# Optimization experiments

Measured on AMD Instinct MI355X. Metric: run time of the kernel, lower is better.

## Reference

```python
import jax, jax.numpy as jnp
import numpy as np

H = 64  # hidden_dim

def _rnn_layer(x, Wih, Whh, bih, bhh):
    # x: [B, T, D_in] -> hidden states [B, T, H]; PyTorch RNN tanh cell:
    # h_t = tanh(W_ih x_t + b_ih + W_hh h_{t-1} + b_hh)
    B = x.shape[0]
    xp = jnp.einsum('btd,hd->bth', x, Wih) + bih  # precompute input projection
    h0 = jnp.zeros((B, H), dtype=x.dtype)
    def step(h, xt):
        h = jnp.tanh(xt + h @ Whh.T + bhh)
        return h, h
    _, hs = jax.lax.scan(step, h0, jnp.swapaxes(xp, 0, 1))  # scan over T
    return jnp.swapaxes(hs, 0, 1)  # [B, T, H]

def setup_inputs() -> dict:
    key = jax.random.key(0)
    ks = jax.random.split(key, 14)
    B, T, D = 4096, 512, 1
    s = 0.1  # small init scale to keep tanh unsaturated
    inp = {
        'x': jax.random.normal(ks[0], (B, T, D), dtype=jnp.float32),
        'W_ih0': jax.random.normal(ks[1], (H, D), dtype=jnp.float32) * s,
        'W_hh0': jax.random.normal(ks[2], (H, H), dtype=jnp.float32) * s,
        'b_ih0': jax.random.normal(ks[3], (H,), dtype=jnp.float32) * s,
        'b_hh0': jax.random.normal(ks[4], (H,), dtype=jnp.float32) * s,
        'W_ih1': jax.random.normal(ks[5], (H, H), dtype=jnp.float32) * s,
        'W_hh1': jax.random.normal(ks[6], (H, H), dtype=jnp.float32) * s,
        'b_ih1': jax.random.normal(ks[7], (H,), dtype=jnp.float32) * s,
        'b_hh1': jax.random.normal(ks[8], (H,), dtype=jnp.float32) * s,
        'fc1_W': jax.random.normal(ks[9], (64, H), dtype=jnp.float32) * s,
        'fc1_b': jax.random.normal(ks[10], (64,), dtype=jnp.float32) * s,
        'fc2_W': jax.random.normal(ks[11], (1, 64), dtype=jnp.float32) * s,
        'fc2_b': jax.random.normal(ks[12], (1,), dtype=jnp.float32) * s,
    }
    return inp

def reference(x, W_ih0, W_hh0, b_ih0, b_hh0, W_ih1, W_hh1, b_ih1, b_hh1,
              fc1_W, fc1_b, fc2_W, fc2_b):
    h1 = _rnn_layer(x, W_ih0, W_hh0, b_ih0, b_hh0)   # layer 0
    h2 = _rnn_layer(h1, W_ih1, W_hh1, b_ih1, b_hh1)  # layer 1
    last = h2[:, -1, :]                               # [B, H]
    z = jax.nn.relu(last @ fc1_W.T + fc1_b)
    return z @ fc2_W.T + fc2_b                        # [B, 1]
```

## Files before the change

### kernel.cpp

```cpp
#include <hip/hip_runtime.h>

namespace {

constexpr int T_LEN = 512;
constexpr int XS    = 516;

typedef _Float16 half8  __attribute__((ext_vector_type(8)));
typedef float    f32x4v __attribute__((ext_vector_type(4)));
typedef unsigned uint2v __attribute__((ext_vector_type(2)));
typedef unsigned uint4v __attribute__((ext_vector_type(4)));

#define MFMA32(a, b, c) __builtin_amdgcn_mfma_f32_16x16x32_f16((a), (b), (c), 0, 0, 0)

constexpr float SCL = 2.8853900817779268f;

__device__ __forceinline__ float exp2_fast(float x) {
#if __has_builtin(__builtin_amdgcn_exp2f)
    return __builtin_amdgcn_exp2f(x);
#else
    return exp2f(x);
#endif
}

__device__ __forceinline__ half8 load_frag(const float* __restrict__ W,
                                           int row, int k0, float s) {
    const float* p = W + row * 64 + k0;
    f32x4v lo = *reinterpret_cast<const f32x4v*>(p);
    f32x4v hi = *reinterpret_cast<const f32x4v*>(p + 4);
    uint4v u;
    u.x = __builtin_bit_cast(unsigned, __builtin_amdgcn_cvt_pkrtz(lo.x * s, lo.y * s));
    u.y = __builtin_bit_cast(unsigned, __builtin_amdgcn_cvt_pkrtz(lo.z * s, lo.w * s));
    u.z = __builtin_bit_cast(unsigned, __builtin_amdgcn_cvt_pkrtz(hi.x * s, hi.y * s));
    u.w = __builtin_bit_cast(unsigned, __builtin_amdgcn_cvt_pkrtz(hi.z * s, hi.w * s));
    return __builtin_bit_cast(half8, u);
}

__device__ __forceinline__ void tanh4(f32x4v &a) {
#pragma unroll
    for (int q = 0; q < 4; ++q) {
        float e = exp2_fast(a[q]);
        a[q] = 1.0f - 2.0f * __builtin_amdgcn_rcpf(e + 1.0f);
    }
}

__device__ __forceinline__ int swz_off(int b, int ro) {
    const int chunk = ro >> 3;
    const int within = ro & 7;
    return (b << 6) + (((chunk ^ (b & 7))) << 3) + within;
}

__global__ __launch_bounds__(256, 2)
void rnn_swz_kernel(const float* __restrict__ x,
                    const float* __restrict__ Wih0,
                    const float* __restrict__ Whh0,
                    const float* __restrict__ bih0,
                    const float* __restrict__ bhh0,
                    const float* __restrict__ Wih1,
                    const float* __restrict__ Whh1,
                    const float* __restrict__ bih1,
                    const float* __restrict__ bhh1,
                    const float* __restrict__ fc1W,
                    const float* __restrict__ fc1b,
                    const float* __restrict__ fc2W,
                    const float* __restrict__ fc2b,
                    float* __restrict__ out)
{
    const int tid    = threadIdx.x;
    const int wv     = tid >> 6;
    const int lane   = tid & 63;
    const int g      = lane >> 4;
    const int b16    = lane & 15;
    const int batch0 = blockIdx.x * 16;

    __shared__ float    sx[16 * XS];
    __shared__ _Float16 sh1[2][16 * 64];
    __shared__ _Float16 sh2[2][16 * 64];
    __shared__ float    pf[4][16];

    {
        const float* gx = x + (size_t)batch0 * T_LEN;
#pragma unroll
        for (int c = 0; c < 8; ++c) {
            int idx = tid + c * 256;
            int r = idx >> 7, c4 = idx & 127;
            f32x4v v = *reinterpret_cast<const f32x4v*>(gx + r * T_LEN + c4 * 4);
            *reinterpret_cast<f32x4v*>(&sx[r * XS + c4 * 4]) = v;
        }
    }

    const int row = 16 * wv + b16;
    const int ro  = 16 * wv + 4 * g;

    const half8 WA0_0 = load_frag(Whh0, row,      8 * g, SCL);
    const half8 WA0_1 = load_frag(Whh0, row, 32 + 8 * g, SCL);
    const half8 WI1_0 = load_frag(Wih1, row,      8 * g, SCL);
    const half8 WI1_1 = load_frag(Wih1, row, 32 + 8 * g, SCL);
    const half8 WH1_0 = load_frag(Whh1, row,      8 * g, SCL);
    const half8 WH1_1 = load_frag(Whh1, row, 32 + 8 * g, SCL);

    f32x4v bb0, bb1, wx2;
#pragma unroll
    for (int q = 0; q < 4; ++q) {
        const int o = 16 * wv + 4 * g + q;
        bb0[q] = SCL * (bih0[o] + bhh0[o]);
        bb1[q] = SCL * (bih1[o] + bhh1[o]);
        wx2[q] = SCL * Wih0[o];
    }

    const int wr_off = swz_off(b16, ro);
    const int rd_b0  = swz_off(b16, 8 * g);
    const int rd_b1  = swz_off(b16, 32 + 8 * g);

    auto publish = [&](_Float16* base, const f32x4v& a) {
        uint2v p;
        p.x = __builtin_bit_cast(unsigned, __builtin_amdgcn_cvt_pkrtz(a[0], a[1]));
        p.y = __builtin_bit_cast(unsigned, __builtin_amdgcn_cvt_pkrtz(a[2], a[3]));
        *reinterpret_cast<uint2v*>(base + wr_off) = p;
    };

    half8 Bh1_0, Bh1_1, Bh2_0, Bh2_1;

    __syncthreads();

    float xt = sx[b16 * XS + 0];
    float xn = sx[b16 * XS + 1];

    {
        f32x4v a0 = wx2 * xt + bb0;
        tanh4(a0);
        publish(sh1[0], a0);
        *reinterpret_cast<uint2v*>(&sh2[0][0] + wr_off) = uint2v{0, 0};
        __syncthreads();
        Bh1_0 = *reinterpret_cast<const half8*>(&sh1[0][0] + rd_b0);
        Bh1_1 = *reinterpret_cast<const half8*>(&sh1[0][0] + rd_b1);
        Bh2_0 = *reinterpret_cast<const half8*>(&sh2[0][0] + rd_b0);
        Bh2_1 = *reinterpret_cast<const half8*>(&sh2[0][0] + rd_b1);
        xt = xn; xn = sx[b16 * XS + 2];
    }

#pragma unroll 2
    for (int k = 1; k < T_LEN; ++k) {
        const int s = k & 1;
        const float xf = sx[b16 * XS + k + 2];

        f32x4v zz = {};
        f32x4v u0 = MFMA32(WA0_0, Bh1_0, wx2 * xt + bb0);
        f32x4v v0 = MFMA32(WA0_1, Bh1_1, zz);
        f32x4v u1 = MFMA32(WI1_0, Bh1_0, bb1);
        f32x4v v1 = MFMA32(WH1_0, Bh2_0, zz);
        u1 = MFMA32(WI1_1, Bh1_1, u1);
        v1 = MFMA32(WH1_1, Bh2_1, v1);

        f32x4v a0 = u0 + v0;
        tanh4(a0);
        publish(sh1[s], a0);

        f32x4v a1 = u1 + v1;
        tanh4(a1);
        publish(sh2[s], a1);

        __syncthreads();
        Bh1_0 = *reinterpret_cast<const half8*>(&sh1[s][0] + rd_b0);
        Bh1_1 = *reinterpret_cast<const half8*>(&sh1[s][0] + rd_b1);
        Bh2_0 = *reinterpret_cast<const half8*>(&sh2[s][0] + rd_b0);
        Bh2_1 = *reinterpret_cast<const half8*>(&sh2[s][0] + rd_b1);
        xt = xn; xn = xf;
    }

    {
        f32x4v zz = {};
        f32x4v u1 = MFMA32(WI1_0, Bh1_0, bb1);
        f32x4v v1 = MFMA32(WH1_0, Bh2_0, zz);
        u1 = MFMA32(WI1_1, Bh1_1, u1);
        v1 = MFMA32(WH1_1, Bh2_1, v1);
        f32x4v a1 = u1 + v1;
        tanh4(a1);
        publish(sh2[0], a1);
        __syncthreads();
        Bh2_0 = *reinterpret_cast<const half8*>(&sh2[0][0] + rd_b0);
        Bh2_1 = *reinterpret_cast<const half8*>(&sh2[0][0] + rd_b1);
    }

    {
        const half8 F0 = load_frag(fc1W, row,      8 * g, 1.0f);
        const half8 F1 = load_frag(fc1W, row, 32 + 8 * g, 1.0f);
        f32x4v zf;
#pragma unroll
        for (int q = 0; q < 4; ++q) zf[q] = fc1b[16 * wv + 4 * g + q];
        zf = MFMA32(F0, Bh2_0, zf);
        zf = MFMA32(F1, Bh2_1, zf);

        float pacc = 0.0f;
#pragma unroll
        for (int q = 0; q < 4; ++q)
            pacc += fmaxf(zf[q], 0.0f) * fc2W[16 * wv + 4 * g + q];
        pacc += __shfl_xor(pacc, 16);
        pacc += __shfl_xor(pacc, 32);
        if (lane < 16) pf[wv][lane] = pacc;
    }
    __syncthreads();
    if (tid < 16)
        out[batch0 + tid] = pf[0][tid] + pf[1][tid] + pf[2][tid] + pf[3][tid]
                          + fc2b[0];
}

}

extern "C" void kernel_launch(void* const* d_in, const int* in_sizes, int n_in,
                              void* d_out, int out_size, void* d_ws, size_t ws_size,
                              hipStream_t stream) {
    (void)n_in; (void)out_size; (void)d_ws; (void)ws_size;
    const float* x    = (const float*)d_in[0];
    const float* Wih0 = (const float*)d_in[1];
    const float* Whh0 = (const float*)d_in[2];
    const float* bih0 = (const float*)d_in[3];
    const float* bhh0 = (const float*)d_in[4];
    const float* Wih1 = (const float*)d_in[5];
    const float* Whh1 = (const float*)d_in[6];
    const float* bih1 = (const float*)d_in[7];
    const float* bhh1 = (const float*)d_in[8];
    const float* fc1W = (const float*)d_in[9];
    const float* fc1b = (const float*)d_in[10];
    const float* fc2W = (const float*)d_in[11];
    const float* fc2b = (const float*)d_in[12];
    float* out = (float*)d_out;

    const int B = in_sizes[0] / T_LEN;
    dim3 grid(B / 16), block(256);
    rnn_swz_kernel<<<grid, block, 0, stream>>>(
        x, Wih0, Whh0, bih0, bhh0, Wih1, Whh1, bih1, bhh1,
        fc1W, fc1b, fc2W, fc2b, out);
}
```

Baseline: 132.5 us.

## Split batch columns across paired waves with 512-thread blocks

Doubles the block to eight waves. Two waves share each output quarter, and each publishes tanh results only for its own half of the 16 batch columns. The MFMA work is duplicated in both waves while the activation and LDS traffic are split by lane predicate. The aim is more waves per SIMD to hide the latency of the serial MFMA → tanh → barrier chain. The cost is redundant matrix work, lane divergence that does not shorten execution, and barriers spanning twice as many waves.

```diff
diff --git a/kernel.cpp b/kernel.cpp
--- a/kernel.cpp
+++ b/kernel.cpp
@@ -46,30 +46,33 @@
 __device__ __forceinline__ int swz_off(int b, int ro) {
     const int chunk = ro >> 3;
     const int within = ro & 7;
-    return (b << 6) + (((chunk ^ (b & 7))) << 3) + within;
-}
-
-__global__ __launch_bounds__(256, 2)
-void rnn_swz_kernel(const float* __restrict__ x,
-                    const float* __restrict__ Wih0,
-                    const float* __restrict__ Whh0,
-                    const float* __restrict__ bih0,
-                    const float* __restrict__ bhh0,
-                    const float* __restrict__ Wih1,
-                    const float* __restrict__ Whh1,
-                    const float* __restrict__ bih1,
-                    const float* __restrict__ bhh1,
-                    const float* __restrict__ fc1W,
-                    const float* __restrict__ fc1b,
-                    const float* __restrict__ fc2W,
-                    const float* __restrict__ fc2b,
-                    float* __restrict__ out)
+    return (b << 6) + ((chunk ^ (b & 7)) << 3) + within;
+}
+
+__global__ __launch_bounds__(512, 1)
+void rnn_hh_kernel(const float* __restrict__ x,
+                   const float* __restrict__ Wih0,
+                   const float* __restrict__ Whh0,
+                   const float* __restrict__ bih0,
+                   const float* __restrict__ bhh0,
+                   const float* __restrict__ Wih1,
+                   const float* __restrict__ Whh1,
+                   const float* __restrict__ bih1,
+                   const float* __restrict__ bhh1,
+                   const float* __restrict__ fc1W,
+                   const float* __restrict__ fc1b,
+                   const float* __restrict__ fc2W,
+                   const float* __restrict__ fc2b,
+                   float* __restrict__ out)
 {
     const int tid    = threadIdx.x;
-    const int wv     = tid >> 6;
+    const int w      = tid >> 6;
+    const int q      = w & 3;
+    const int hh     = w >> 2;
     const int lane   = tid & 63;
     const int g      = lane >> 4;
     const int b16    = lane & 15;
+    const bool own   = ((b16 >> 3) == hh);
     const int batch0 = blockIdx.x * 16;
 
     __shared__ float    sx[16 * XS];
@@ -80,16 +83,16 @@
     {
         const float* gx = x + (size_t)batch0 * T_LEN;
 #pragma unroll
-        for (int c = 0; c < 8; ++c) {
-            int idx = tid + c * 256;
+        for (int c = 0; c < 4; ++c) {
+            int idx = tid + c * 512;
             int r = idx >> 7, c4 = idx & 127;
             f32x4v v = *reinterpret_cast<const f32x4v*>(gx + r * T_LEN + c4 * 4);
             *reinterpret_cast<f32x4v*>(&sx[r * XS + c4 * 4]) = v;
         }
     }
 
-    const int row = 16 * wv + b16;
-    const int ro  = 16 * wv + 4 * g;
+    const int row = 16 * q + b16;
+    const int ro  = 16 * q + 4 * g;
 
     const half8 WA0_0 = load_frag(Whh0, row,      8 * g, SCL);
     const half8 WA0_1 = load_frag(Whh0, row, 32 + 8 * g, SCL);
@@ -100,11 +103,11 @@
 
     f32x4v bb0, bb1, wx2;
 #pragma unroll
-    for (int q = 0; q < 4; ++q) {
-        const int o = 16 * wv + 4 * g + q;
-        bb0[q] = SCL * (bih0[o] + bhh0[o]);
-        bb1[q] = SCL * (bih1[o] + bhh1[o]);
-        wx2[q] = SCL * Wih0[o];
+    for (int iq = 0; iq < 4; ++iq) {
+        const int o = 16 * q + 4 * g + iq;
+        bb0[iq] = SCL * (bih0[o] + bhh0[o]);
+        bb1[iq] = SCL * (bih1[o] + bhh1[o]);
+        wx2[iq] = SCL * Wih0[o];
     }
 
     const int wr_off = swz_off(b16, ro);
@@ -118,7 +121,7 @@
         *reinterpret_cast<uint2v*>(base + wr_off) = p;
     };
 
-    half8 Bh1_0, Bh1_1, Bh2_0, Bh2_1;
+    half8 Bh1_0 = {}, Bh1_1 = {}, Bh2_0 = {}, Bh2_1 = {};
 
     __syncthreads();
 
@@ -127,14 +130,18 @@
 
     {
         f32x4v a0 = wx2 * xt + bb0;
-        tanh4(a0);
-        publish(sh1[0], a0);
-        *reinterpret_cast<uint2v*>(&sh2[0][0] + wr_off) = uint2v{0, 0};
+        if (own) {
+            tanh4(a0);
+            publish(sh1[0], a0);
+            *reinterpret_cast<uint2v*>(&sh2[0][0] + wr_off) = uint2v{0, 0};
+        }
         __syncthreads();
-        Bh1_0 = *reinterpret_cast<const half8*>(&sh1[0][0] + rd_b0);
-        Bh1_1 = *reinterpret_cast<const half8*>(&sh1[0][0] + rd_b1);
-        Bh2_0 = *reinterpret_cast<const half8*>(&sh2[0][0] + rd_b0);
-        Bh2_1 = *reinterpret_cast<const half8*>(&sh2[0][0] + rd_b1);
+        if (own) {
+            Bh1_0 = *reinterpret_cast<const half8*>(&sh1[0][0] + rd_b0);
+            Bh1_1 = *reinterpret_cast<const half8*>(&sh1[0][0] + rd_b1);
+            Bh2_0 = *reinterpret_cast<const half8*>(&sh2[0][0] + rd_b0);
+            Bh2_1 = *reinterpret_cast<const half8*>(&sh2[0][0] + rd_b1);
+        }
         xt = xn; xn = sx[b16 * XS + 2];
     }
 
@@ -151,19 +158,21 @@
         u1 = MFMA32(WI1_1, Bh1_1, u1);
         v1 = MFMA32(WH1_1, Bh2_1, v1);
 
-        f32x4v a0 = u0 + v0;
-        tanh4(a0);
-        publish(sh1[s], a0);
-
-        f32x4v a1 = u1 + v1;
-        tanh4(a1);
-        publish(sh2[s], a1);
-
+        if (own) {
+            f32x4v a0 = u0 + v0;
+            tanh4(a0);
+            publish(sh1[s], a0);
+            f32x4v a1 = u1 + v1;
+            tanh4(a1);
+            publish(sh2[s], a1);
+        }
         __syncthreads();
-        Bh1_0 = *reinterpret_cast<const half8*>(&sh1[s][0] + rd_b0);
-        Bh1_1 = *reinterpret_cast<const half8*>(&sh1[s][0] + rd_b1);
-        Bh2_0 = *reinterpret_cast<const half8*>(&sh2[s][0] + rd_b0);
-        Bh2_1 = *reinterpret_cast<const half8*>(&sh2[s][0] + rd_b1);
+        if (own) {
+            Bh1_0 = *reinterpret_cast<const half8*>(&sh1[s][0] + rd_b0);
+            Bh1_1 = *reinterpret_cast<const half8*>(&sh1[s][0] + rd_b1);
+            Bh2_0 = *reinterpret_cast<const half8*>(&sh2[s][0] + rd_b0);
+            Bh2_1 = *reinterpret_cast<const half8*>(&sh2[s][0] + rd_b1);
+        }
         xt = xn; xn = xf;
     }
 
@@ -173,30 +182,32 @@
         f32x4v v1 = MFMA32(WH1_0, Bh2_0, zz);
         u1 = MFMA32(WI1_1, Bh1_1, u1);
         v1 = MFMA32(WH1_1, Bh2_1, v1);
-        f32x4v a1 = u1 + v1;
-        tanh4(a1);
-        publish(sh2[0], a1);
+        if (own) {
+            f32x4v a1 = u1 + v1;
+            tanh4(a1);
+            publish(sh2[0], a1);
+        }
         __syncthreads();
-        Bh2_0 = *reinterpret_cast<const half8*>(&sh2[0][0] + rd_b0);
-        Bh2_1 = *reinterpret_cast<const half8*>(&sh2[0][0] + rd_b1);
-    }
-
-    {
+    }
+
+    if (hh == 0) {
+        half8 E0 = *reinterpret_cast<const half8*>(&sh2[0][0] + rd_b0);
+        half8 E1 = *reinterpret_cast<const half8*>(&sh2[0][0] + rd_b1);
         const half8 F0 = load_frag(fc1W, row,      8 * g, 1.0f);
         const half8 F1 = load_frag(fc1W, row, 32 + 8 * g, 1.0f);
         f32x4v zf;
 #pragma unroll
-        for (int q = 0; q < 4; ++q) zf[q] = fc1b[16 * wv + 4 * g + q];
-        zf = MFMA32(F0, Bh2_0, zf);
-        zf = MFMA32(F1, Bh2_1, zf);
+        for (int iq = 0; iq < 4; ++iq) zf[iq] = fc1b[16 * q + 4 * g + iq];
+        zf = MFMA32(F0, E0, zf);
+        zf = MFMA32(F1, E1, zf);
 
         float pacc = 0.0f;
 #pragma unroll
-        for (int q = 0; q < 4; ++q)
-            pacc += fmaxf(zf[q], 0.0f) * fc2W[16 * wv + 4 * g + q];
+        for (int iq = 0; iq < 4; ++iq)
+            pacc += fmaxf(zf[iq], 0.0f) * fc2W[16 * q + 4 * g + iq];
         pacc += __shfl_xor(pacc, 16);
         pacc += __shfl_xor(pacc, 32);
-        if (lane < 16) pf[wv][lane] = pacc;
+        if (lane < 16) pf[q][lane] = pacc;
     }
     __syncthreads();
     if (tid < 16)
@@ -226,8 +237,8 @@
     float* out = (float*)d_out;
 
     const int B = in_sizes[0] / T_LEN;
-    dim3 grid(B / 16), block(256);
-    rnn_swz_kernel<<<grid, block, 0, stream>>>(
+    dim3 grid(B / 16), block(512);
+    rnn_hh_kernel<<<grid, block, 0, stream>>>(
         x, Wih0, Whh0, bih0, bhh0, Wih1, Whh1, bih1, bhh1,
         fc1W, fc1b, fc2W, fc2b, out);
 }
```

Measured after the change: 229.0 us. 72.9% more time.
